# Performance work log

Hardware: AMD Instinct MI355X
Metric: run time of the kernel (lower is better)

Reference implementation:

```python
import jax, jax.numpy as jnp
import numpy as np

N_NODES = 100000
N_EDGES = 1600000
DIM = 128
N_LAYERS = 3
BN_EPS = 1e-5


def setup_inputs() -> dict:
    key = jax.random.key(0)
    ks = jax.random.split(key, 2 + 2 * N_LAYERS)
    x = jax.random.normal(ks[0], (N_NODES, DIM), dtype=jnp.float32)
    edge_index = jax.random.randint(ks[1], (2, N_EDGES), 0, N_NODES, dtype=jnp.int32)
    Ws = tuple(jax.random.normal(ks[2 + i], (DIM, DIM), dtype=jnp.float32) * 0.05
               for i in range(N_LAYERS))
    bs = tuple(jax.random.normal(ks[2 + N_LAYERS + i], (DIM,), dtype=jnp.float32) * 0.05
               for i in range(N_LAYERS))
    gammas = tuple(jnp.ones((DIM,), jnp.float32) for _ in range(N_LAYERS))
    betas = tuple(jnp.zeros((DIM,), jnp.float32) for _ in range(N_LAYERS))
    return {"x": x, "edge_index": edge_index, "Ws": Ws, "bs": bs,
            "gammas": gammas, "betas": betas}


def _gnn_forward(x, edge_index, Ws, bs, gammas, betas):
    # GCNConv (PyG semantics): add self loops, symmetric D^-1/2 (A+I) D^-1/2 norm,
    # message = norm * (x @ W)[src], scatter-add to dst, + bias.
    n = x.shape[0]
    loops = jnp.arange(n, dtype=edge_index.dtype)
    src = jnp.concatenate([edge_index[0], loops])
    dst = jnp.concatenate([edge_index[1], loops])
    deg = jax.ops.segment_sum(jnp.ones(src.shape[0], x.dtype), dst, num_segments=n)
    dinv = jnp.where(deg > 0, jax.lax.rsqrt(deg), 0.0)
    norm = dinv[src] * dinv[dst]  # [E+N]

    h = x
    prev = None
    for i in range(N_LAYERS):
        xw = h @ Ws[i]                                   # [N, H]
        msg = xw[src] * norm[:, None]                    # gather + scale
        out = jax.ops.segment_sum(msg, dst, num_segments=n) + bs[i]
        if i > 0:  # residual only when shapes match (layers 1..)
            out = out + prev
        # BatchNorm1d over node dim (training-mode batch statistics, biased var)
        mu = out.mean(axis=0)
        var = out.var(axis=0)
        out = (out - mu) * jax.lax.rsqrt(var + BN_EPS) * gammas[i] + betas[i]
        out = jax.nn.relu(out)
        # dropout: identity (eval / deterministic reference)
        prev = out
        h = out
    return h


def reference(x, edge_index, Ws, bs, gammas, betas):
    return _gnn_forward(x, edge_index, Ws, bs, gammas, betas)
```

## Files before the change

### kernel.cpp

```cpp
#include <hip/hip_runtime.h>

#define DIM 128
#define BN_EPS 1e-5f
#define SCAN_BS 512
typedef unsigned int u32;
typedef __attribute__((ext_vector_type(8))) short short8;
typedef __attribute__((ext_vector_type(4))) float f32x4;

__device__ __forceinline__ u32 bf16rne(float x) {
  u32 u = __float_as_uint(x);
  return (u + 0x7FFFu + ((u >> 16) & 1u)) >> 16;
}
__device__ __forceinline__ float bflo(u32 u) { return __uint_as_float(u << 16); }
__device__ __forceinline__ float bfhi(u32 u) { return __uint_as_float(u & 0xFFFF0000u); }


__global__ __launch_bounds__(256) void k_count(const int* __restrict__ dst,
                                               int* __restrict__ ideg, int ne) {
  int stride = gridDim.x * blockDim.x;
  for (int e = blockIdx.x * blockDim.x + threadIdx.x; e < ne; e += stride)
    atomicAdd(&ideg[dst[e]], 1);
}


__global__ __launch_bounds__(SCAN_BS) void k_scan1(const int* __restrict__ ideg,
                                                   int* __restrict__ bsum, int n) {
  __shared__ int red[SCAN_BS];
  int t = threadIdx.x;
  int i = blockIdx.x * SCAN_BS + t;
  red[t] = (i < n) ? ideg[i] : 0;
  __syncthreads();
  for (int d = SCAN_BS / 2; d > 0; d >>= 1) {
    if (t < d) red[t] += red[t + d];
    __syncthreads();
  }
  if (t == 0) bsum[blockIdx.x] = red[0];
}

__global__ __launch_bounds__(256) void k_scan2(const int* __restrict__ bsum,
                                               int* __restrict__ bbase, int nb,
                                               int* __restrict__ off, int n, int ne) {
  __shared__ int s[256];
  int t = threadIdx.x;
  s[t] = (t < nb) ? bsum[t] : 0;
  __syncthreads();
  for (int d = 1; d < 256; d <<= 1) {
    int v = (t >= d) ? s[t - d] : 0;
    __syncthreads();
    s[t] += v;
    __syncthreads();
  }
  if (t < nb) bbase[t] = (t == 0) ? 0 : s[t - 1];
  if (t == 0) off[n] = ne;
}

__global__ __launch_bounds__(SCAN_BS) void k_scan3(const int* __restrict__ ideg,
                                                   const int* __restrict__ bbase,
                                                   int* __restrict__ off,
                                                   int* __restrict__ cur,
                                                   float* __restrict__ dinv, int n) {
  __shared__ int s[SCAN_BS];
  int t = threadIdx.x;
  int i = blockIdx.x * SCAN_BS + t;
  int v = (i < n) ? ideg[i] : 0;
  s[t] = v;
  __syncthreads();
  for (int d = 1; d < SCAN_BS; d <<= 1) {
    int u = (t >= d) ? s[t - d] : 0;
    __syncthreads();
    s[t] += u;
    __syncthreads();
  }
  if (i < n) {
    int excl = bbase[blockIdx.x] + s[t] - v;
    off[i] = excl;
    cur[i] = excl;
    dinv[i] = rsqrtf((float)v + 1.0f);
  }
}

__global__ __launch_bounds__(256) void k_fill(const int* __restrict__ src,
                                              const int* __restrict__ dst,
                                              int* __restrict__ cur,
                                              int* __restrict__ csr_src, int ne) {
  int stride = gridDim.x * blockDim.x;
  for (int e = blockIdx.x * blockDim.x + threadIdx.x; e < ne; e += stride) {
    int d = dst[e];
    int s = src[e];
    int p = atomicAdd(&cur[d], 1);
    csr_src[p] = s;
  }
}


__global__ __launch_bounds__(256) void k_wprep(const float* __restrict__ W0,
                                               const float* __restrict__ W1,
                                               const float* __restrict__ W2,
                                               u32* __restrict__ Wt) {
  const float* W = blockIdx.x == 0 ? W0 : (blockIdx.x == 1 ? W1 : W2);
  u32* o = Wt + (size_t)blockIdx.x * DIM * 64;
  int tid = threadIdx.x;
#pragma unroll
  for (int i = 0; i < 32; ++i) {
    int u = tid + i * 256;
    int c = u >> 6;
    int kk = u & 63;
    float lo = W[(size_t)(2 * kk) * DIM + c];
    float hi = W[(size_t)(2 * kk + 1) * DIM + c];
    o[u] = bf16rne(lo) | (bf16rne(hi) << 16);
  }
}


__global__ __launch_bounds__(256) void k_gemm(const float* __restrict__ A,
                                              const u32* __restrict__ Wt,
                                              const float* __restrict__ dinv,
                                              const float* __restrict__ sc,
                                              const float* __restrict__ sh,
                                              u32* __restrict__ C, int n) {
  __shared__ u32 sA[8192];
  __shared__ u32 sB[8192];
  __shared__ float sdv[DIM];
  int tid = threadIdx.x;
  int row0 = blockIdx.x * DIM;

  {
    const uint4* w4 = (const uint4*)Wt;
#pragma unroll
    for (int i = 0; i < 8; ++i) {
      int u = tid + i * 256;
      int r = u >> 4, s = u & 15;
      uint4 v = w4[u];
      ((uint4*)sB)[r * 16 + (s ^ (r & 7))] = v;
    }
  }
#pragma unroll
  for (int i = 0; i < 8; ++i) {
    int u = tid + i * 256;
    int r = u >> 4, s = u & 15;
    int gr = row0 + r;
    uint4 pv = make_uint4(0u, 0u, 0u, 0u);
    if (gr < n) {
      float4 v0 = ((const float4*)A)[(size_t)gr * 32 + s * 2];
      float4 v1 = ((const float4*)A)[(size_t)gr * 32 + s * 2 + 1];
      if (sc) {
        float4 s0 = ((const float4*)sc)[s * 2];
        float4 s1 = ((const float4*)sc)[s * 2 + 1];
        float4 h0 = ((const float4*)sh)[s * 2];
        float4 h1 = ((const float4*)sh)[s * 2 + 1];
        v0.x = fmaxf(fmaf(v0.x, s0.x, h0.x), 0.f);
        v0.y = fmaxf(fmaf(v0.y, s0.y, h0.y), 0.f);
        v0.z = fmaxf(fmaf(v0.z, s0.z, h0.z), 0.f);
        v0.w = fmaxf(fmaf(v0.w, s0.w, h0.w), 0.f);
        v1.x = fmaxf(fmaf(v1.x, s1.x, h1.x), 0.f);
        v1.y = fmaxf(fmaf(v1.y, s1.y, h1.y), 0.f);
        v1.z = fmaxf(fmaf(v1.z, s1.z, h1.z), 0.f);
        v1.w = fmaxf(fmaf(v1.w, s1.w, h1.w), 0.f);
      }
      pv.x = bf16rne(v0.x) | (bf16rne(v0.y) << 16);
      pv.y = bf16rne(v0.z) | (bf16rne(v0.w) << 16);
      pv.z = bf16rne(v1.x) | (bf16rne(v1.y) << 16);
      pv.w = bf16rne(v1.z) | (bf16rne(v1.w) << 16);
    }
    ((uint4*)sA)[r * 16 + (s ^ (r & 7))] = pv;
  }
  if (tid < DIM) sdv[tid] = (row0 + tid < n) ? dinv[row0 + tid] : 0.f;
  __syncthreads();

  int lane = tid & 63;
  int w = tid >> 6;
  int lr = lane & 15;
  int g = lane >> 4;
  f32x4 acc[2][8];
#pragma unroll
  for (int m = 0; m < 2; ++m)
#pragma unroll
    for (int nt = 0; nt < 8; ++nt) acc[m][nt] = (f32x4){0.f, 0.f, 0.f, 0.f};

#pragma unroll
  for (int kc = 0; kc < 4; ++kc) {
    short8 a[2], b[8];
#pragma unroll
    for (int m = 0; m < 2; ++m) {
      int r = w * 32 + m * 16 + lr;
      int sp = (kc * 4 + g) ^ (r & 7);
      a[m] = *(const short8*)&sA[(r * 16 + sp) * 4];
    }
#pragma unroll
    for (int nt = 0; nt < 8; ++nt) {
      int r = nt * 16 + lr;
      int sp = (kc * 4 + g) ^ (r & 7);
      b[nt] = *(const short8*)&sB[(r * 16 + sp) * 4];
    }
#pragma unroll
    for (int m = 0; m < 2; ++m)
#pragma unroll
      for (int nt = 0; nt < 8; ++nt)
        acc[m][nt] = __builtin_amdgcn_mfma_f32_16x16x32_bf16(a[m], b[nt], acc[m][nt], 0, 0, 0);
  }
  __syncthreads();

  {
    unsigned short* so = (unsigned short*)sA;
#pragma unroll
    for (int m = 0; m < 2; ++m) {
#pragma unroll
      for (int nt = 0; nt < 8; ++nt) {
#pragma unroll
        for (int r4 = 0; r4 < 4; ++r4) {
          int rl = w * 32 + m * 16 + g * 4 + r4;
          int col = ((nt ^ ((rl >> 2) & 7)) << 4) + lr;
          so[rl * DIM + col] = (unsigned short)bf16rne(acc[m][nt][r4] * sdv[rl]);
        }
      }
    }
  }
  __syncthreads();
#pragma unroll
  for (int i = 0; i < 8; ++i) {
    int u = tid + i * 256;
    int r = u >> 4, s = u & 15;
    if (row0 + r < n) {
      int sswz = (s & 1) | (((s >> 1) ^ ((r >> 2) & 7)) << 1);
      ((uint4*)C)[(size_t)(row0 + r) * 16 + s] = ((uint4*)sA)[r * 16 + sswz];
    }
  }
}


__global__ __launch_bounds__(256) void k_agg(const u32* __restrict__ xw,
                                             const int* __restrict__ off,
                                             const int* __restrict__ csr_src,
                                             const float* __restrict__ dinv,
                                             const float* __restrict__ bias,
                                             const float* __restrict__ prev,
                                             const float* __restrict__ psc,
                                             const float* __restrict__ psh,
                                             float* __restrict__ out,
                                             float* __restrict__ ssum,
                                             float* __restrict__ ssq, int n) {
  int tid = threadIdx.x;
  int lane = tid & 63;
  int wave = tid >> 6;
  float2 bc = ((const float2*)bias)[lane];
  float2 ps, ph;
  if (psc) {
    ps = ((const float2*)psc)[lane];
    ph = ((const float2*)psh)[lane];
  }
  float s0 = 0.f, s1 = 0.f, q0 = 0.f, q1 = 0.f;
  int stride = gridDim.x * 4;

  for (int node = blockIdx.x * 4 + wave; node < n; node += stride) {
    int e0 = __builtin_amdgcn_readfirstlane(off[node]);
    int e1 = __builtin_amdgcn_readfirstlane(off[node + 1]);
    float a0, a1;
    {
      u32 s = xw[(size_t)node * 64 + lane];
      a0 = bflo(s);
      a1 = bfhi(s);
    }
    int e = e0;
    for (; e + 8 <= e1; e += 8) {
      int i0 = __builtin_amdgcn_readfirstlane(csr_src[e]);
      int i1 = __builtin_amdgcn_readfirstlane(csr_src[e + 1]);
      int i2 = __builtin_amdgcn_readfirstlane(csr_src[e + 2]);
      int i3 = __builtin_amdgcn_readfirstlane(csr_src[e + 3]);
      int i4 = __builtin_amdgcn_readfirstlane(csr_src[e + 4]);
      int i5 = __builtin_amdgcn_readfirstlane(csr_src[e + 5]);
      int i6 = __builtin_amdgcn_readfirstlane(csr_src[e + 6]);
      int i7 = __builtin_amdgcn_readfirstlane(csr_src[e + 7]);
      u32 v0 = xw[(size_t)i0 * 64 + lane];
      u32 v1 = xw[(size_t)i1 * 64 + lane];
      u32 v2 = xw[(size_t)i2 * 64 + lane];
      u32 v3 = xw[(size_t)i3 * 64 + lane];
      u32 v4 = xw[(size_t)i4 * 64 + lane];
      u32 v5 = xw[(size_t)i5 * 64 + lane];
      u32 v6 = xw[(size_t)i6 * 64 + lane];
      u32 v7 = xw[(size_t)i7 * 64 + lane];
      a0 += ((bflo(v0) + bflo(v1)) + (bflo(v2) + bflo(v3))) +
            ((bflo(v4) + bflo(v5)) + (bflo(v6) + bflo(v7)));
      a1 += ((bfhi(v0) + bfhi(v1)) + (bfhi(v2) + bfhi(v3))) +
            ((bfhi(v4) + bfhi(v5)) + (bfhi(v6) + bfhi(v7)));
    }
    for (; e + 4 <= e1; e += 4) {
      int i0 = __builtin_amdgcn_readfirstlane(csr_src[e]);
      int i1 = __builtin_amdgcn_readfirstlane(csr_src[e + 1]);
      int i2 = __builtin_amdgcn_readfirstlane(csr_src[e + 2]);
      int i3 = __builtin_amdgcn_readfirstlane(csr_src[e + 3]);
      u32 v0 = xw[(size_t)i0 * 64 + lane];
      u32 v1 = xw[(size_t)i1 * 64 + lane];
      u32 v2 = xw[(size_t)i2 * 64 + lane];
      u32 v3 = xw[(size_t)i3 * 64 + lane];
      a0 += (bflo(v0) + bflo(v1)) + (bflo(v2) + bflo(v3));
      a1 += (bfhi(v0) + bfhi(v1)) + (bfhi(v2) + bfhi(v3));
    }
    for (; e < e1; ++e) {
      int i0 = __builtin_amdgcn_readfirstlane(csr_src[e]);
      u32 v = xw[(size_t)i0 * 64 + lane];
      a0 += bflo(v);
      a1 += bfhi(v);
    }
    float di = dinv[node];
    float v0 = fmaf(di, a0, bc.x);
    float v1 = fmaf(di, a1, bc.y);
    if (prev) {
      float2 pv = ((const float2*)prev)[(size_t)node * 64 + lane];
      if (psc) {
        pv.x = fmaxf(fmaf(pv.x, ps.x, ph.x), 0.f);
        pv.y = fmaxf(fmaf(pv.y, ps.y, ph.y), 0.f);
      }
      v0 += pv.x;
      v1 += pv.y;
    }
    ((float2*)out)[(size_t)node * 64 + lane] = make_float2(v0, v1);
    s0 += v0;
    s1 += v1;
    q0 = fmaf(v0, v0, q0);
    q1 = fmaf(v1, v1, q1);
  }

  __shared__ float red[4][64][2];
  red[wave][lane][0] = s0;
  red[wave][lane][1] = s1;
  __syncthreads();
  if (wave == 0) {
    float t0 = (red[0][lane][0] + red[1][lane][0]) + (red[2][lane][0] + red[3][lane][0]);
    float t1 = (red[0][lane][1] + red[1][lane][1]) + (red[2][lane][1] + red[3][lane][1]);
    atomicAdd(&ssum[lane * 2], t0);
    atomicAdd(&ssum[lane * 2 + 1], t1);
  }
  __syncthreads();
  red[wave][lane][0] = q0;
  red[wave][lane][1] = q1;
  __syncthreads();
  if (wave == 0) {
    float t0 = (red[0][lane][0] + red[1][lane][0]) + (red[2][lane][0] + red[3][lane][0]);
    float t1 = (red[0][lane][1] + red[1][lane][1]) + (red[2][lane][1] + red[3][lane][1]);
    atomicAdd(&ssq[lane * 2], t0);
    atomicAdd(&ssq[lane * 2 + 1], t1);
  }
}


__global__ void k_bn(const float* __restrict__ ssum, const float* __restrict__ ssq,
                     const float* __restrict__ gamma, const float* __restrict__ beta,
                     float* __restrict__ scale, float* __restrict__ shift, float invn) {
  int c = threadIdx.x;
  float mu = ssum[c] * invn;
  float var = ssq[c] * invn - mu * mu;
  float rstd = rsqrtf(var + BN_EPS);
  float s = rstd * gamma[c];
  scale[c] = s;
  shift[c] = beta[c] - mu * s;
}

__global__ __launch_bounds__(256) void k_norm(const float* __restrict__ in,
                                              float* __restrict__ out,
                                              const float* __restrict__ scale,
                                              const float* __restrict__ shift, int n4) {
  int stride = gridDim.x * blockDim.x;
  for (int i = blockIdx.x * blockDim.x + threadIdx.x; i < n4; i += stride) {
    int cg = i & 31;
    float4 sc = ((const float4*)scale)[cg];
    float4 sh = ((const float4*)shift)[cg];
    float4 v = ((const float4*)in)[i];
    v.x = fmaxf(fmaf(v.x, sc.x, sh.x), 0.f);
    v.y = fmaxf(fmaf(v.y, sc.y, sh.y), 0.f);
    v.z = fmaxf(fmaf(v.z, sc.z, sh.z), 0.f);
    v.w = fmaxf(fmaf(v.w, sc.w, sh.w), 0.f);
    ((float4*)out)[i] = v;
  }
}


extern "C" void kernel_launch(void* const* d_in, const int* in_sizes, int n_in,
                              void* d_out, int out_size, void* d_ws, size_t ws_size,
                              hipStream_t stream) {
  const float* x = (const float*)d_in[0];
  const int* ei = (const int*)d_in[1];
  int n = in_sizes[0] / DIM;
  int ne = in_sizes[1] / 2;
  const int* src = ei;
  const int* dst = ei + ne;

  const float *W[3], *B[3], *G[3], *Bt[3];
  if (n_in >= 14) {
    for (int l = 0; l < 3; ++l) {
      W[l] = (const float*)d_in[2 + l];
      B[l] = (const float*)d_in[5 + l];
      G[l] = (const float*)d_in[8 + l];
      Bt[l] = (const float*)d_in[11 + l];
    }
  } else {
    for (int l = 0; l < 3; ++l) {
      W[l] = (const float*)d_in[2] + (size_t)l * DIM * DIM;
      B[l] = (const float*)d_in[3] + (size_t)l * DIM;
      G[l] = (const float*)d_in[4] + (size_t)l * DIM;
      Bt[l] = (const float*)d_in[5] + (size_t)l * DIM;
    }
  }

  float* out = (float*)d_out;

  char* p = (char*)d_ws;
  auto carve = [&](size_t bytes) {
    void* q = (void*)p;
    p += (bytes + 255) & ~(size_t)255;
    return q;
  };
  int* ideg = (int*)carve((size_t)n * 4);
  int* coff = (int*)carve((size_t)(n + 1) * 4);
  int* cur = (int*)carve((size_t)n * 4);
  float* dinv = (float*)carve((size_t)n * 4);
  int* csr_src = (int*)carve((size_t)ne * 4);
  u32* xw = (u32*)carve((size_t)n * DIM * 2);
  float* buf1 = (float*)carve((size_t)n * DIM * 4);
  u32* wt = (u32*)carve(3 * DIM * 64 * 4);
  float* stats = (float*)carve(3 * 256 * 4);
  float* scsh = (float*)carve(3 * 256 * 4);
  int* bsum = (int*)carve(256 * 4);
  int* bbase = (int*)carve(256 * 4);

  hipMemsetAsync(ideg, 0, (size_t)n * 4, stream);
  hipMemsetAsync(stats, 0, 3 * 256 * 4, stream);

  int nscan = (n + SCAN_BS - 1) / SCAN_BS;

  k_wprep<<<3, 256, 0, stream>>>(W[0], W[1], W[2], wt);
  k_count<<<1024, 256, 0, stream>>>(dst, ideg, ne);
  k_scan1<<<nscan, SCAN_BS, 0, stream>>>(ideg, bsum, n);
  k_scan2<<<1, 256, 0, stream>>>(bsum, bbase, nscan, coff, n, ne);
  k_scan3<<<nscan, SCAN_BS, 0, stream>>>(ideg, bbase, coff, cur, dinv, n);
  k_fill<<<1024, 256, 0, stream>>>(src, dst, cur, csr_src, ne);

  float invn = 1.0f / (float)n;
  int nblk = (n + DIM - 1) / DIM;
  const int AGG_GRID = 2048;

  float* ss0 = stats;         float* sc0 = scsh;
  k_gemm<<<nblk, 256, 0, stream>>>(x, wt, dinv, nullptr, nullptr, xw, n);
  k_agg<<<AGG_GRID, 256, 0, stream>>>(xw, coff, csr_src, dinv, B[0], nullptr, nullptr, nullptr,
                                      buf1, ss0, ss0 + 128, n);
  k_bn<<<1, 128, 0, stream>>>(ss0, ss0 + 128, G[0], Bt[0], sc0, sc0 + 128, invn);

  float* ss1 = stats + 256;   float* sc1 = scsh + 256;
  k_gemm<<<nblk, 256, 0, stream>>>(buf1, wt + (size_t)DIM * 64, dinv, sc0, sc0 + 128, xw, n);
  k_agg<<<AGG_GRID, 256, 0, stream>>>(xw, coff, csr_src, dinv, B[1], buf1, sc0, sc0 + 128,
                                      out, ss1, ss1 + 128, n);
  k_bn<<<1, 128, 0, stream>>>(ss1, ss1 + 128, G[1], Bt[1], sc1, sc1 + 128, invn);

  float* ss2 = stats + 512;   float* sc2 = scsh + 512;
  k_gemm<<<nblk, 256, 0, stream>>>(out, wt + (size_t)2 * DIM * 64, dinv, sc1, sc1 + 128, xw, n);
  k_agg<<<AGG_GRID, 256, 0, stream>>>(xw, coff, csr_src, dinv, B[2], out, sc1, sc1 + 128,
                                      buf1, ss2, ss2 + 128, n);
  k_bn<<<1, 128, 0, stream>>>(ss2, ss2 + 128, G[2], Bt[2], sc2, sc2 + 128, invn);

  k_norm<<<2048, 256, 0, stream>>>(buf1, out, sc2, sc2 + 128, n * DIM / 4);
}
```

Measured before the change: 774.7 us.

## Store pre-BN layer outputs in bf16 and fold BN finalize into consumers

The intermediate pre-BatchNorm layer outputs are now stored as packed bf16 instead of fp32, which halves the bytes written by aggregation and read back by the next GEMM, residual add and final normalize. The separate single-block BN-finalize kernels are removed; each consumer (GEMM, aggregation, final normalize) recomputes the per-channel scale and shift from the raw sum and sum-of-squares statistics. This saves three small launches and the traffic through an fp32 buffer, but adds bf16 rounding on the residual path and the final output, plus redundant rsqrt work per thread.

```diff
diff --git a/kernel.cpp b/kernel.cpp
--- a/kernel.cpp
+++ b/kernel.cpp
@@ -13,6 +13,7 @@
 }
 __device__ __forceinline__ float bflo(u32 u) { return __uint_as_float(u << 16); }
 __device__ __forceinline__ float bfhi(u32 u) { return __uint_as_float(u & 0xFFFF0000u); }
+__device__ __forceinline__ u32 pk(float a, float b) { return bf16rne(a) | (bf16rne(b) << 16); }
 
 
 __global__ __launch_bounds__(256) void k_count(const int* __restrict__ dst,
@@ -21,7 +22,6 @@
   for (int e = blockIdx.x * blockDim.x + threadIdx.x; e < ne; e += stride)
     atomicAdd(&ideg[dst[e]], 1);
 }
-
 
 __global__ __launch_bounds__(SCAN_BS) void k_scan1(const int* __restrict__ ideg,
                                                    int* __restrict__ bsum, int n) {
@@ -107,23 +107,37 @@
     int kk = u & 63;
     float lo = W[(size_t)(2 * kk) * DIM + c];
     float hi = W[(size_t)(2 * kk + 1) * DIM + c];
-    o[u] = bf16rne(lo) | (bf16rne(hi) << 16);
-  }
-}
-
-
-__global__ __launch_bounds__(256) void k_gemm(const float* __restrict__ A,
+    o[u] = pk(lo, hi);
+  }
+}
+
+
+__global__ __launch_bounds__(256) void k_gemm(const float* __restrict__ Af,
+                                              const u32* __restrict__ Abf,
                                               const u32* __restrict__ Wt,
                                               const float* __restrict__ dinv,
-                                              const float* __restrict__ sc,
-                                              const float* __restrict__ sh,
+                                              const float* __restrict__ ssum,
+                                              const float* __restrict__ ssq,
+                                              const float* __restrict__ gamma,
+                                              const float* __restrict__ beta,
+                                              float invn,
                                               u32* __restrict__ C, int n) {
   __shared__ u32 sA[8192];
   __shared__ u32 sB[8192];
   __shared__ float sdv[DIM];
+  __shared__ float ssc[DIM];
+  __shared__ float ssh[DIM];
   int tid = threadIdx.x;
   int row0 = blockIdx.x * DIM;
 
+  if (Abf && tid < DIM) {
+    float mu = ssum[tid] * invn;
+    float var = ssq[tid] * invn - mu * mu;
+    float rstd = rsqrtf(var + BN_EPS);
+    float s = rstd * gamma[tid];
+    ssc[tid] = s;
+    ssh[tid] = beta[tid] - mu * s;
+  }
   {
     const uint4* w4 = (const uint4*)Wt;
 #pragma unroll
@@ -134,6 +148,8 @@
       ((uint4*)sB)[r * 16 + (s ^ (r & 7))] = v;
     }
   }
+  if (Abf) __syncthreads();
+
 #pragma unroll
   for (int i = 0; i < 8; ++i) {
     int u = tid + i * 256;
@@ -141,26 +157,29 @@
     int gr = row0 + r;
     uint4 pv = make_uint4(0u, 0u, 0u, 0u);
     if (gr < n) {
-      float4 v0 = ((const float4*)A)[(size_t)gr * 32 + s * 2];
-      float4 v1 = ((const float4*)A)[(size_t)gr * 32 + s * 2 + 1];
-      if (sc) {
-        float4 s0 = ((const float4*)sc)[s * 2];
-        float4 s1 = ((const float4*)sc)[s * 2 + 1];
-        float4 h0 = ((const float4*)sh)[s * 2];
-        float4 h1 = ((const float4*)sh)[s * 2 + 1];
-        v0.x = fmaxf(fmaf(v0.x, s0.x, h0.x), 0.f);
-        v0.y = fmaxf(fmaf(v0.y, s0.y, h0.y), 0.f);
-        v0.z = fmaxf(fmaf(v0.z, s0.z, h0.z), 0.f);
-        v0.w = fmaxf(fmaf(v0.w, s0.w, h0.w), 0.f);
-        v1.x = fmaxf(fmaf(v1.x, s1.x, h1.x), 0.f);
-        v1.y = fmaxf(fmaf(v1.y, s1.y, h1.y), 0.f);
-        v1.z = fmaxf(fmaf(v1.z, s1.z, h1.z), 0.f);
-        v1.w = fmaxf(fmaf(v1.w, s1.w, h1.w), 0.f);
+      if (Abf) {
+        uint4 v = ((const uint4*)Abf)[(size_t)gr * 16 + s];
+        int c = s * 8;
+        float f0 = fmaxf(fmaf(bflo(v.x), ssc[c + 0], ssh[c + 0]), 0.f);
+        float f1 = fmaxf(fmaf(bfhi(v.x), ssc[c + 1], ssh[c + 1]), 0.f);
+        float f2 = fmaxf(fmaf(bflo(v.y), ssc[c + 2], ssh[c + 2]), 0.f);
+        float f3 = fmaxf(fmaf(bfhi(v.y), ssc[c + 3], ssh[c + 3]), 0.f);
+        float f4 = fmaxf(fmaf(bflo(v.z), ssc[c + 4], ssh[c + 4]), 0.f);
+        float f5 = fmaxf(fmaf(bfhi(v.z), ssc[c + 5], ssh[c + 5]), 0.f);
+        float f6 = fmaxf(fmaf(bflo(v.w), ssc[c + 6], ssh[c + 6]), 0.f);
+        float f7 = fmaxf(fmaf(bfhi(v.w), ssc[c + 7], ssh[c + 7]), 0.f);
+        pv.x = pk(f0, f1);
+        pv.y = pk(f2, f3);
+        pv.z = pk(f4, f5);
+        pv.w = pk(f6, f7);
+      } else {
+        float4 v0 = ((const float4*)Af)[(size_t)gr * 32 + s * 2];
+        float4 v1 = ((const float4*)Af)[(size_t)gr * 32 + s * 2 + 1];
+        pv.x = pk(v0.x, v0.y);
+        pv.y = pk(v0.z, v0.w);
+        pv.z = pk(v1.x, v1.y);
+        pv.w = pk(v1.z, v1.w);
       }
-      pv.x = bf16rne(v0.x) | (bf16rne(v0.y) << 16);
-      pv.y = bf16rne(v0.z) | (bf16rne(v0.w) << 16);
-      pv.z = bf16rne(v1.x) | (bf16rne(v1.y) << 16);
-      pv.w = bf16rne(v1.z) | (bf16rne(v1.w) << 16);
     }
     ((uint4*)sA)[r * 16 + (s ^ (r & 7))] = pv;
   }
@@ -233,10 +252,13 @@
                                              const int* __restrict__ csr_src,
                                              const float* __restrict__ dinv,
                                              const float* __restrict__ bias,
-                                             const float* __restrict__ prev,
-                                             const float* __restrict__ psc,
-                                             const float* __restrict__ psh,
-                                             float* __restrict__ out,
+                                             const u32* __restrict__ prev,
+                                             const float* __restrict__ psum,
+                                             const float* __restrict__ psq,
+                                             const float* __restrict__ pgam,
+                                             const float* __restrict__ pbet,
+                                             float invn,
+                                             u32* __restrict__ out,
                                              float* __restrict__ ssum,
                                              float* __restrict__ ssq, int n) {
   int tid = threadIdx.x;
@@ -244,9 +266,15 @@
   int wave = tid >> 6;
   float2 bc = ((const float2*)bias)[lane];
   float2 ps, ph;
-  if (psc) {
-    ps = ((const float2*)psc)[lane];
-    ph = ((const float2*)psh)[lane];
+  if (prev) {
+    int c0 = lane * 2, c1 = c0 + 1;
+    float m0 = psum[c0] * invn, m1 = psum[c1] * invn;
+    float r0 = rsqrtf(psq[c0] * invn - m0 * m0 + BN_EPS);
+    float r1 = rsqrtf(psq[c1] * invn - m1 * m1 + BN_EPS);
+    ps.x = r0 * pgam[c0];
+    ps.y = r1 * pgam[c1];
+    ph.x = pbet[c0] - m0 * ps.x;
+    ph.y = pbet[c1] - m1 * ps.y;
   }
   float s0 = 0.f, s1 = 0.f, q0 = 0.f, q1 = 0.f;
   int stride = gridDim.x * 4;
@@ -305,15 +333,11 @@
     float v0 = fmaf(di, a0, bc.x);
     float v1 = fmaf(di, a1, bc.y);
     if (prev) {
-      float2 pv = ((const float2*)prev)[(size_t)node * 64 + lane];
-      if (psc) {
-        pv.x = fmaxf(fmaf(pv.x, ps.x, ph.x), 0.f);
-        pv.y = fmaxf(fmaf(pv.y, ps.y, ph.y), 0.f);
-      }
-      v0 += pv.x;
-      v1 += pv.y;
-    }
-    ((float2*)out)[(size_t)node * 64 + lane] = make_float2(v0, v1);
+      u32 pv = prev[(size_t)node * 64 + lane];
+      v0 += fmaxf(fmaf(bflo(pv), ps.x, ph.x), 0.f);
+      v1 += fmaxf(fmaf(bfhi(pv), ps.y, ph.y), 0.f);
+    }
+    out[(size_t)node * 64 + lane] = pk(v0, v1);
     s0 += v0;
     s1 += v1;
     q0 = fmaf(v0, v0, q0);
@@ -343,33 +367,37 @@
 }
 
 
-__global__ void k_bn(const float* __restrict__ ssum, const float* __restrict__ ssq,
-                     const float* __restrict__ gamma, const float* __restrict__ beta,
-                     float* __restrict__ scale, float* __restrict__ shift, float invn) {
-  int c = threadIdx.x;
-  float mu = ssum[c] * invn;
-  float var = ssq[c] * invn - mu * mu;
-  float rstd = rsqrtf(var + BN_EPS);
-  float s = rstd * gamma[c];
-  scale[c] = s;
-  shift[c] = beta[c] - mu * s;
-}
-
-__global__ __launch_bounds__(256) void k_norm(const float* __restrict__ in,
+__global__ __launch_bounds__(256) void k_norm(const u32* __restrict__ in,
                                               float* __restrict__ out,
-                                              const float* __restrict__ scale,
-                                              const float* __restrict__ shift, int n4) {
+                                              const float* __restrict__ ssum,
+                                              const float* __restrict__ ssq,
+                                              const float* __restrict__ gamma,
+                                              const float* __restrict__ beta,
+                                              float invn, int n32) {
   int stride = gridDim.x * blockDim.x;
-  for (int i = blockIdx.x * blockDim.x + threadIdx.x; i < n4; i += stride) {
-    int cg = i & 31;
-    float4 sc = ((const float4*)scale)[cg];
-    float4 sh = ((const float4*)shift)[cg];
-    float4 v = ((const float4*)in)[i];
-    v.x = fmaxf(fmaf(v.x, sc.x, sh.x), 0.f);
-    v.y = fmaxf(fmaf(v.y, sc.y, sh.y), 0.f);
-    v.z = fmaxf(fmaf(v.z, sc.z, sh.z), 0.f);
-    v.w = fmaxf(fmaf(v.w, sc.w, sh.w), 0.f);
-    ((float4*)out)[i] = v;
+  for (int j = blockIdx.x * blockDim.x + threadIdx.x; j < n32; j += stride) {
+    int cg = j & 31;
+    float4 sm = ((const float4*)ssum)[cg];
+    float4 sq = ((const float4*)ssq)[cg];
+    float4 g = ((const float4*)gamma)[cg];
+    float4 b = ((const float4*)beta)[cg];
+    float4 mu = make_float4(sm.x * invn, sm.y * invn, sm.z * invn, sm.w * invn);
+    float4 sc, sh;
+    sc.x = rsqrtf(sq.x * invn - mu.x * mu.x + BN_EPS) * g.x;
+    sc.y = rsqrtf(sq.y * invn - mu.y * mu.y + BN_EPS) * g.y;
+    sc.z = rsqrtf(sq.z * invn - mu.z * mu.z + BN_EPS) * g.z;
+    sc.w = rsqrtf(sq.w * invn - mu.w * mu.w + BN_EPS) * g.w;
+    sh.x = b.x - mu.x * sc.x;
+    sh.y = b.y - mu.y * sc.y;
+    sh.z = b.z - mu.z * sc.z;
+    sh.w = b.w - mu.w * sc.w;
+    uint2 v = ((const uint2*)in)[j];
+    float4 o;
+    o.x = fmaxf(fmaf(bflo(v.x), sc.x, sh.x), 0.f);
+    o.y = fmaxf(fmaf(bfhi(v.x), sc.y, sh.y), 0.f);
+    o.z = fmaxf(fmaf(bflo(v.y), sc.z, sh.z), 0.f);
+    o.w = fmaxf(fmaf(bfhi(v.y), sc.w, sh.w), 0.f);
+    ((float4*)out)[j] = o;
   }
 }
 
@@ -415,10 +443,10 @@
   float* dinv = (float*)carve((size_t)n * 4);
   int* csr_src = (int*)carve((size_t)ne * 4);
   u32* xw = (u32*)carve((size_t)n * DIM * 2);
-  float* buf1 = (float*)carve((size_t)n * DIM * 4);
+  u32* rawA = (u32*)carve((size_t)n * DIM * 2);
+  u32* rawB = (u32*)carve((size_t)n * DIM * 2);
   u32* wt = (u32*)carve(3 * DIM * 64 * 4);
   float* stats = (float*)carve(3 * 256 * 4);
-  float* scsh = (float*)carve(3 * 256 * 4);
   int* bsum = (int*)carve(256 * 4);
   int* bbase = (int*)carve(256 * 4);
 
@@ -438,23 +466,27 @@
   int nblk = (n + DIM - 1) / DIM;
   const int AGG_GRID = 2048;
 
-  float* ss0 = stats;         float* sc0 = scsh;
-  k_gemm<<<nblk, 256, 0, stream>>>(x, wt, dinv, nullptr, nullptr, xw, n);
-  k_agg<<<AGG_GRID, 256, 0, stream>>>(xw, coff, csr_src, dinv, B[0], nullptr, nullptr, nullptr,
-                                      buf1, ss0, ss0 + 128, n);
-  k_bn<<<1, 128, 0, stream>>>(ss0, ss0 + 128, G[0], Bt[0], sc0, sc0 + 128, invn);
-
-  float* ss1 = stats + 256;   float* sc1 = scsh + 256;
-  k_gemm<<<nblk, 256, 0, stream>>>(buf1, wt + (size_t)DIM * 64, dinv, sc0, sc0 + 128, xw, n);
-  k_agg<<<AGG_GRID, 256, 0, stream>>>(xw, coff, csr_src, dinv, B[1], buf1, sc0, sc0 + 128,
-                                      out, ss1, ss1 + 128, n);
-  k_bn<<<1, 128, 0, stream>>>(ss1, ss1 + 128, G[1], Bt[1], sc1, sc1 + 128, invn);
-
-  float* ss2 = stats + 512;   float* sc2 = scsh + 512;
-  k_gemm<<<nblk, 256, 0, stream>>>(out, wt + (size_t)2 * DIM * 64, dinv, sc1, sc1 + 128, xw, n);
-  k_agg<<<AGG_GRID, 256, 0, stream>>>(xw, coff, csr_src, dinv, B[2], out, sc1, sc1 + 128,
-                                      buf1, ss2, ss2 + 128, n);
-  k_bn<<<1, 128, 0, stream>>>(ss2, ss2 + 128, G[2], Bt[2], sc2, sc2 + 128, invn);
-
-  k_norm<<<2048, 256, 0, stream>>>(buf1, out, sc2, sc2 + 128, n * DIM / 4);
-}
+  float* ss0 = stats;
+  float* ss1 = stats + 256;
+  float* ss2 = stats + 512;
+
+  k_gemm<<<nblk, 256, 0, stream>>>(x, nullptr, wt, dinv,
+                                   nullptr, nullptr, nullptr, nullptr, 0.f, xw, n);
+  k_agg<<<AGG_GRID, 256, 0, stream>>>(xw, coff, csr_src, dinv, B[0], nullptr,
+                                      nullptr, nullptr, nullptr, nullptr, invn,
+                                      rawA, ss0, ss0 + 128, n);
+
+  k_gemm<<<nblk, 256, 0, stream>>>(nullptr, rawA, wt + (size_t)DIM * 64, dinv,
+                                   ss0, ss0 + 128, G[0], Bt[0], invn, xw, n);
+  k_agg<<<AGG_GRID, 256, 0, stream>>>(xw, coff, csr_src, dinv, B[1], rawA,
+                                      ss0, ss0 + 128, G[0], Bt[0], invn,
+                                      rawB, ss1, ss1 + 128, n);
+
+  k_gemm<<<nblk, 256, 0, stream>>>(nullptr, rawB, wt + (size_t)2 * DIM * 64, dinv,
+                                   ss1, ss1 + 128, G[1], Bt[1], invn, xw, n);
+  k_agg<<<AGG_GRID, 256, 0, stream>>>(xw, coff, csr_src, dinv, B[2], rawB,
+                                      ss1, ss1 + 128, G[1], Bt[1], invn,
+                                      rawA, ss2, ss2 + 128, n);
+
+  k_norm<<<2048, 256, 0, stream>>>(rawA, out, ss2, ss2 + 128, G[2], Bt[2], invn, n * 32);
+}
```

Measured after the change: 758.8 us. 1.02x faster.
